# Kernel optimization log

Measured on AMD Instinct MI355X. Metric: run time of the kernel, lower is better.

Reference implementation:

```python
import jax, jax.numpy as jnp
import numpy as np

D_MODEL = 1024
N_HEADS = 16
HEAD_DIM = D_MODEL // N_HEADS
SEQ = 4096
BATCH = 4


def setup_inputs() -> dict:
    key = jax.random.key(0)
    ks = jax.random.split(key, 10)
    s = 0.02
    inp = {
        "h": jax.random.normal(ks[0], (SEQ, BATCH, D_MODEL), jnp.float32),
        "x": jax.random.normal(ks[1], (SEQ, BATCH, D_MODEL), jnp.float32),
        "Wq": jax.random.normal(ks[2], (D_MODEL, D_MODEL), jnp.float32) * s,
        "bq": jnp.zeros((D_MODEL,), jnp.float32),
        "Wk": jax.random.normal(ks[3], (D_MODEL, D_MODEL), jnp.float32) * s,
        "bk": jnp.zeros((D_MODEL,), jnp.float32),
        "Wv": jax.random.normal(ks[4], (D_MODEL, D_MODEL), jnp.float32) * s,
        "bv": jnp.zeros((D_MODEL,), jnp.float32),
        "Wo": jax.random.normal(ks[5], (D_MODEL, D_MODEL), jnp.float32) * s,
        "bo": jnp.zeros((D_MODEL,), jnp.float32),
    }
    return inp


def _heads(t):
    # [S, B, D] -> [B, H, S, d]
    S, B, _ = t.shape
    return t.reshape(S, B, N_HEADS, HEAD_DIM).transpose(1, 2, 0, 3)


def reference(h, x, Wq, bq, Wk, bk, Wv, bv, Wo, bo):
    # torch Linear: y = x @ W.T + b
    Q = _heads(h @ Wq.T + bq)
    K = _heads(x @ Wk.T + bk)
    V = _heads(x @ Wv.T + bv)
    Qp = jax.nn.elu(Q) + 1.0
    Kp = jax.nn.elu(K) + 1.0
    KV = jnp.einsum('bhsd,bhsv->bhdv', Kp, V)          # [B,H,d,d]
    K_sum = Kp.sum(axis=2)                              # [B,H,d]
    Z = jnp.einsum('bhsd,bhd->bhs', Qp, K_sum) + 1e-6   # [B,H,S]
    out = jnp.einsum('bhsd,bhdv->bhsv', Qp, KV) / Z[..., None]
    # [B,H,S,d] -> [S,B,D]
    S, B = h.shape[0], h.shape[1]
    out = out.transpose(2, 0, 1, 3).reshape(S, B, D_MODEL)
    return out @ Wo.T + bo
```

## Files before the change

### kernel.cpp

```cpp
#include <hip/hip_runtime.h>
#include <hip/hip_bf16.h>
#include <cstdint>
#include <cstddef>

#define S_LEN   4096
#define BATCHN  4
#define DMODEL  1024
#define NHEADS  16
#define HDIM    64
#define MROWS   (S_LEN*BATCHN)
#define KDIM    1024
#define NTK     (KDIM/32)
#define CLP     136

typedef __bf16 bf16;
typedef bf16 bf16x8 __attribute__((ext_vector_type(8)));
typedef bf16 bf16x4 __attribute__((ext_vector_type(4)));
typedef float f32x4 __attribute__((ext_vector_type(4)));

#define MFMA16(a,b,c) __builtin_amdgcn_mfma_f32_16x16x32_bf16(a,b,c,0,0,0)

__device__ __forceinline__ void gll16(const void* g, void* l) {
  __builtin_amdgcn_global_load_lds((const __attribute__((address_space(1))) unsigned*)g,
                                   (__attribute__((address_space(3))) unsigned*)l,
                                   16, 0, 0);
}

__global__ __launch_bounds__(256) void cast_perm(const float* __restrict__ h,
                                                 const float* __restrict__ x,
                                                 bf16* __restrict__ hb,
                                                 bf16* __restrict__ xb) {
  const int n = MROWS * KDIM;
  int stride = gridDim.x * blockDim.x * 4;
  for (int i = (blockIdx.x * blockDim.x + threadIdx.x) * 4; i < n; i += stride) {
    int s = i >> 12, b = (i >> 10) & 3, d = i & 1023;
    size_t o = ((size_t)(b * S_LEN + s) << 10) | d;
    float4 f = *(const float4*)(h + i);
    bf16x4 u; u[0]=(bf16)f.x; u[1]=(bf16)f.y; u[2]=(bf16)f.z; u[3]=(bf16)f.w;
    *(bf16x4*)(hb + o) = u;
    float4 g = *(const float4*)(x + i);
    bf16x4 v; v[0]=(bf16)g.x; v[1]=(bf16)g.y; v[2]=(bf16)g.z; v[3]=(bf16)g.w;
    *(bf16x4*)(xb + o) = v;
  }
}

__global__ __launch_bounds__(256) void cast_w(const float* __restrict__ Wq,
                                              const float* __restrict__ Wk,
                                              const float* __restrict__ Wv,
                                              const float* __restrict__ Wo,
                                              bf16* __restrict__ dst) {
  const int n = 4 * 1048576;
  int stride = gridDim.x * blockDim.x * 4;
  for (int i = (blockIdx.x * blockDim.x + threadIdx.x) * 4; i < n; i += stride) {
    int r = i >> 20;
    const float* src = (r < 1) ? (Wq + i) : (r < 2) ? (Wk + i - 1048576)
                     : (r < 3) ? (Wv + i - 2097152) : (Wo + i - 3145728);
    float4 f = *(const float4*)src;
    bf16x4 o; o[0]=(bf16)f.x; o[1]=(bf16)f.y; o[2]=(bf16)f.z; o[3]=(bf16)f.w;
    *(bf16x4*)(dst + i) = o;
  }
}

struct GemmAcc { f32x4 a[4][4]; };

__device__ __forceinline__ void gemm_tile(const bf16* __restrict__ A,
                                          const bf16* __restrict__ Bw,
                                          size_t arow0, size_t brow0,
                                          bf16* sm, GemmAcc& G) {
  const int tid  = threadIdx.x;
  const int wid  = tid >> 6;
  const int lane = tid & 63;
  const int wm = wid >> 1, wn = wid & 1;
  const int lr = lane >> 2;
  const int lc = lane & 3;
  const int ssrc = (((lc << 4) ^ (((lr >> 1) & 3) << 4)) >> 1);
  const int fhalf = (lane >> 4) << 4;

  const bf16* ap[2]; const bf16* bp[2]; int sdo[2];
  #pragma unroll
  for (int i = 0; i < 2; ++i) {
    int seg = (wid << 1) | i;
    ap[i] = A  + (arow0 + seg*16 + lr) * KDIM + ssrc;
    bp[i] = Bw + (brow0 + seg*16 + lr) * KDIM + ssrc;
    sdo[i] = seg * 512;
  }

  #pragma unroll
  for (int i = 0; i < 2; ++i) { gll16(ap[i],      sm + sdo[i]); gll16(bp[i],      sm + 4096 + sdo[i]); }
  #pragma unroll
  for (int i = 0; i < 2; ++i) { gll16(ap[i] + 32, sm + 8192 + sdo[i]); gll16(bp[i] + 32, sm + 12288 + sdo[i]); }
  asm volatile("s_waitcnt vmcnt(4)" ::: "memory");
  __builtin_amdgcn_s_barrier();
  asm volatile("" ::: "memory");

  int cur = 0;
  for (int t = 0; t < NTK; ++t) {
    const bf16* As = sm + cur * 8192;
    const bf16* Bs = As + 4096;

    bf16x8 af[4], bfv[4];
    #pragma unroll
    for (int m = 0; m < 4; ++m) {
      int R = wm*64 + m*16 + (lane & 15);
      af[m] = *(const bf16x8*)((const char*)As + R*64 + (fhalf ^ (((R >> 1) & 3) << 4)));
    }
    #pragma unroll
    for (int n = 0; n < 4; ++n) {
      int R = wn*64 + n*16 + (lane & 15);
      bfv[n] = *(const bf16x8*)((const char*)Bs + R*64 + (fhalf ^ (((R >> 1) & 3) << 4)));
    }

    if (t + 2 < NTK) {
      int nx2 = cur + 2; if (nx2 >= 3) nx2 -= 3;
      bf16* wbA = sm + nx2 * 8192;
      const int ko = (t + 2) * 32;
      #pragma unroll
      for (int i = 0; i < 2; ++i) {
        gll16(ap[i] + ko, wbA + sdo[i]);
        gll16(bp[i] + ko, wbA + 4096 + sdo[i]);
      }
    }

    #pragma unroll
    for (int m = 0; m < 4; ++m)
      #pragma unroll
      for (int n = 0; n < 4; ++n)
        G.a[m][n] = MFMA16(af[m], bfv[n], G.a[m][n]);

    if (t < NTK - 2)       asm volatile("s_waitcnt vmcnt(4)" ::: "memory");
    else if (t == NTK - 2) asm volatile("s_waitcnt vmcnt(0)" ::: "memory");
    if (t < NTK - 1) {
      __builtin_amdgcn_s_barrier();
      asm volatile("" ::: "memory");
    }
    cur = (cur == 2) ? 0 : cur + 1;
  }
}

template<int MODE>
__global__ __launch_bounds__(256) void gemm_bt(
    const bf16* __restrict__ A, const bf16* __restrict__ Bw,
    const float* __restrict__ bias0,
    void* __restrict__ Cout) {
  __shared__ __align__(16) bf16 sm[3 * 8192];
  const int tid  = threadIdx.x;
  const int wid  = tid >> 6;
  const int lane = tid & 63;
  const int wm = wid >> 1, wn = wid & 1;
  const int mtile = blockIdx.x, ntile = blockIdx.y;

  GemmAcc G = {};
  gemm_tile(A, Bw, (size_t)mtile * 128, (size_t)ntile * 128, sm, G);

  #pragma unroll
  for (int m = 0; m < 4; ++m) {
    int rowb = mtile*128 + wm*64 + m*16 + ((lane >> 4) << 2);
    #pragma unroll
    for (int n = 0; n < 4; ++n) {
      int col = ntile*128 + wn*64 + n*16 + (lane & 15);
      float bias = bias0[col];
      if (MODE == 0) {
        bf16* C = (bf16*)Cout;
        #pragma unroll
        for (int i = 0; i < 4; ++i) {
          float v = G.a[m][n][i] + bias;
          v = (v > 0.f) ? v + 1.f : __expf(v);
          C[(size_t)(rowb+i)*DMODEL + col] = (bf16)v;
        }
      } else {
        float* C = (float*)Cout;
        #pragma unroll
        for (int i = 0; i < 4; ++i)
          C[(size_t)(rowb+i)*DMODEL + col] = G.a[m][n][i] + bias;
      }
    }
  }
}

__global__ __launch_bounds__(512, 4) void kvproj(
    const bf16* __restrict__ Wkv, const bf16* __restrict__ xb,
    const float* __restrict__ bk, const float* __restrict__ bv,
    float* __restrict__ kvb, float* __restrict__ ksb) {
  __shared__ __align__(16) bf16 sm[3 * 12288];
  const int tid  = threadIdx.x;
  const int wid  = tid >> 6;
  const int lane = tid & 63;
  const int wm = wid >> 1, wn = wid & 1;
  const int m = blockIdx.x, ntile = blockIdx.y;
  const int lr = lane >> 2;
  const int lc = lane & 3;
  const int ssrc = (((lc << 4) ^ (((lr >> 1) & 3) << 4)) >> 1);
  const int fhalf = (lane >> 4) << 4;

  const bf16* KA = Wkv + (size_t)(m * 128) * KDIM;
  const bf16* VA = Wkv + (size_t)(1024 + m * 128) * KDIM;
  const bf16* BB = xb + (size_t)(ntile * 128) * KDIM;

  const bf16* ap[2]; const bf16* bp; int sda[2], sdb;
  #pragma unroll
  for (int i = 0; i < 2; ++i) {
    int seg = (wid << 1) | i;
    const bf16* base = (seg < 8) ? KA : VA;
    ap[i] = base + (size_t)((seg & 7) * 16 + lr) * KDIM + ssrc;
    sda[i] = seg * 512;
  }
  bp = BB + (size_t)(wid * 16 + lr) * KDIM + ssrc;
  sdb = 8192 + wid * 512;

  #pragma unroll
  for (int i = 0; i < 2; ++i) gll16(ap[i], sm + sda[i]);
  gll16(bp, sm + sdb);
  #pragma unroll
  for (int i = 0; i < 2; ++i) gll16(ap[i] + 32, sm + 12288 + sda[i]);
  gll16(bp + 32, sm + 12288 + sdb);
  asm volatile("s_waitcnt vmcnt(3)" ::: "memory");
  __builtin_amdgcn_s_barrier();
  asm volatile("" ::: "memory");

  f32x4 acc[4][4] = {};
  int cur = 0;
  for (int t = 0; t < NTK; ++t) {
    const bf16* As = sm + cur * 12288;
    const bf16* Bs = As + 8192;

    bf16x8 af[4], bfv[4];
    #pragma unroll
    for (int mm = 0; mm < 4; ++mm) {
      int R = wm*64 + mm*16 + (lane & 15);
      af[mm] = *(const bf16x8*)((const char*)As + R*64 + (fhalf ^ (((R >> 1) & 3) << 4)));
    }
    #pragma unroll
    for (int nn = 0; nn < 4; ++nn) {
      int R = wn*64 + nn*16 + (lane & 15);
      bfv[nn] = *(const bf16x8*)((const char*)Bs + R*64 + (fhalf ^ (((R >> 1) & 3) << 4)));
    }

    if (t + 2 < NTK) {
      int nx2 = cur + 2; if (nx2 >= 3) nx2 -= 3;
      bf16* wb = sm + nx2 * 12288;
      const int ko = (t + 2) * 32;
      #pragma unroll
      for (int i = 0; i < 2; ++i) gll16(ap[i] + ko, wb + sda[i]);
      gll16(bp + ko, wb + sdb);
    }

    #pragma unroll
    for (int mm = 0; mm < 4; ++mm)
      #pragma unroll
      for (int nn = 0; nn < 4; ++nn)
        acc[mm][nn] = MFMA16(af[mm], bfv[nn], acc[mm][nn]);

    if (t < NTK - 2)       asm volatile("s_waitcnt vmcnt(3)" ::: "memory");
    else if (t == NTK - 2) asm volatile("s_waitcnt vmcnt(0)" ::: "memory");
    if (t < NTK - 1) {
      __builtin_amdgcn_s_barrier();
      asm volatile("" ::: "memory");
    }
    cur = (cur == 2) ? 0 : cur + 1;
  }
  __syncthreads();

  bf16* CL = sm;
  #pragma unroll
  for (int mm = 0; mm < 4; ++mm) {
    #pragma unroll
    for (int i = 0; i < 4; ++i) {
      int ra = wm*64 + mm*16 + ((lane >> 4) << 2) + i;
      float bias = (ra < 128) ? bk[m*128 + ra] : bv[m*128 + ra - 128];
      #pragma unroll
      for (int nn = 0; nn < 4; ++nn) {
        int cb = wn*64 + nn*16 + (lane & 15);
        float v = acc[mm][nn][i] + bias;
        if (ra < 128) v = (v > 0.f) ? v + 1.f : __expf(v);
        CL[ra*CLP + cb] = (bf16)v;
      }
    }
  }
  __syncthreads();

  const int hl = wid >> 2;
  const int ww = wid & 3;
  const int bh = (ntile >> 5) * 16 + 2*m + hl;
  f32x4 acc2[4] = {};
  #pragma unroll
  for (int ks = 0; ks < 4; ++ks) {
    bf16x8 akv = *(const bf16x8*)(CL + (hl*64 + ww*16 + (lane & 15))*CLP + ks*32 + ((lane >> 4) << 3));
    #pragma unroll
    for (int nn = 0; nn < 4; ++nn) {
      bf16x8 bkv = *(const bf16x8*)(CL + (128 + hl*64 + nn*16 + (lane & 15))*CLP + ks*32 + ((lane >> 4) << 3));
      acc2[nn] = MFMA16(akv, bkv, acc2[nn]);
    }
  }
  float* KVh = kvb + (size_t)bh * 4096;
  #pragma unroll
  for (int nn = 0; nn < 4; ++nn)
    #pragma unroll
    for (int i = 0; i < 4; ++i) {
      int dd = ww*16 + ((lane >> 4) << 2) + i;
      int vv = nn*16 + (lane & 15);
      atomicAdd(&KVh[dd*64 + vv], acc2[nn][i]);
    }

  {
    int rid = tid >> 2, part = tid & 3;
    float s = 0.f;
    #pragma unroll
    for (int j = 0; j < 32; ++j) s += (float)CL[rid*CLP + part*32 + j];
    s += __shfl_xor(s, 1);
    s += __shfl_xor(s, 2);
    if (part == 0) {
      int hh = rid >> 6, d = rid & 63;
      atomicAdd(&ksb[((ntile >> 5) * 16 + 2*m + hh)*64 + d], s);
    }
  }
}

__global__ __launch_bounds__(256) void attn_out(const bf16* __restrict__ QP,
                                                const float* __restrict__ KVg,
                                                const float* __restrict__ Ksumg,
                                                bf16* __restrict__ OP) {
  const int head = blockIdx.x, stile = blockIdx.y;
  const int b = head >> 4, hh = head & 15;
  const int tid = threadIdx.x;
  const int wid = tid >> 6, lane = tid & 63;
  const int s0 = stile * 128;
  __shared__ __align__(16) bf16 Qs[128*64];
  __shared__ __align__(16) bf16 KVt[64*64];
  __shared__ float ksum_s[64];
  __shared__ float rZ[128];

  const float* KVh = KVg + (size_t)head*4096;
  #pragma unroll
  for (int i = 0; i < 16; ++i) {
    int idx = i*256 + tid;
    int dd = idx >> 6, vv = idx & 63;
    KVt[vv*64 + dd] = (bf16)KVh[idx];
  }
  if (tid < 64) ksum_s[tid] = Ksumg[head*64 + tid];
  #pragma unroll
  for (int p = 0; p < 4; ++p) {
    int row = p*32 + wid*8 + (lane >> 3);
    gll16(QP + ((size_t)(b*S_LEN + s0 + row))*DMODEL + hh*64 + ((lane&7)<<3),
          Qs + (p*32 + wid*8)*64);
  }
  __syncthreads();

  if (tid < 128) {
    float z = 0.f;
    #pragma unroll
    for (int dd = 0; dd < 64; ++dd) z += (float)Qs[tid*64 + dd] * ksum_s[dd];
    rZ[tid] = 1.f / (z + 1e-6f);
  }
  __syncthreads();

  f32x4 acc[2][4] = {};
  #pragma unroll
  for (int ksb2 = 0; ksb2 < 2; ++ksb2) {
    bf16x8 af[2], bv[4];
    #pragma unroll
    for (int m = 0; m < 2; ++m)
      af[m] = *(const bf16x8*)(Qs + (wid*32 + m*16 + (lane & 15))*64 + ksb2*32 + ((lane>>4)<<3));
    #pragma unroll
    for (int n = 0; n < 4; ++n)
      bv[n] = *(const bf16x8*)(KVt + (n*16 + (lane & 15))*64 + ksb2*32 + ((lane>>4)<<3));
    #pragma unroll
    for (int m = 0; m < 2; ++m)
      #pragma unroll
      for (int n = 0; n < 4; ++n)
        acc[m][n] = MFMA16(af[m], bv[n], acc[m][n]);
  }

  #pragma unroll
  for (int m = 0; m < 2; ++m)
    #pragma unroll
    for (int n = 0; n < 4; ++n)
      #pragma unroll
      for (int i = 0; i < 4; ++i) {
        int row = wid*32 + m*16 + ((lane >> 4) << 2) + i;
        int vv  = n*16 + (lane & 15);
        float val = acc[m][n][i] * rZ[row];
        OP[((size_t)((s0+row)*BATCHN + b))*DMODEL + hh*64 + vv] = (bf16)val;
      }
}

extern "C" void kernel_launch(void* const* d_in, const int* in_sizes, int n_in,
                              void* d_out, int out_size, void* d_ws, size_t ws_size,
                              hipStream_t stream) {
  const float* h  = (const float*)d_in[0];
  const float* x  = (const float*)d_in[1];
  const float* Wq = (const float*)d_in[2];
  const float* bq = (const float*)d_in[3];
  const float* Wk = (const float*)d_in[4];
  const float* bk = (const float*)d_in[5];
  const float* Wv = (const float*)d_in[6];
  const float* bv = (const float*)d_in[7];
  const float* Wo = (const float*)d_in[8];
  const float* bo = (const float*)d_in[9];

  char* ws = (char*)d_ws;
  bf16*  hb   = (bf16*)(ws);
  bf16*  xb   = (bf16*)(ws + 33554432);
  bf16*  wcat = (bf16*)(ws + 67108864);
  bf16*  wob  = (bf16*)(ws + 73400320);
  bf16*  qp   = (bf16*)(ws + 75497472);
  float* kvb  = (float*)(ws + 109051904);
  float* ksb  = (float*)(ws + 110100480);
  bf16*  op   = (bf16*)(ws + 110116864);

  cast_perm<<<dim3(4096), 256, 0, stream>>>(h, x, hb, xb);
  cast_w<<<dim3(2048), 256, 0, stream>>>(Wq, Wk, Wv, Wo, wcat);

  hipMemsetAsync(kvb, 0, 1048576 + 16384, stream);

  kvproj<<<dim3(8, 128), 512, 0, stream>>>(wcat + 1048576, xb, bk, bv, kvb, ksb);
  gemm_bt<0><<<dim3(128, 8), 256, 0, stream>>>(hb, wcat, bq, qp);
  attn_out<<<dim3(64, 32), 256, 0, stream>>>(qp, kvb, ksb, op);
  gemm_bt<2><<<dim3(128, 8), 256, 0, stream>>>(op, wob, bo, d_out);
}
```

Before: 257.1 us.

## Fold per-head KV state into output weights and fuse normalizer into Q GEMM

Replaces the per-head attention-output kernel with a small GEMM that premultiplies Wo by each batch/head KV matrix, giving a per-batch combined weight. The Q projection epilogue now computes the feature map, the Z normalizer via cross-lane shuffles, and the scaled Qp. The output GEMM then consumes the normalized Q directly with the batch-specific fused weight. This removes the attn_out pass and its intermediate read/write of the activations. In exchange it adds a weight-sized per-batch precompute and rounds KV·Wo to bf16, which changes numerics.

```diff
diff --git a/kernel.cpp b/kernel.cpp
--- a/kernel.cpp
+++ b/kernel.cpp
@@ -137,11 +137,10 @@
   }
 }
 
-template<int MODE>
-__global__ __launch_bounds__(256) void gemm_bt(
+__global__ __launch_bounds__(256) void q_gemm(
     const bf16* __restrict__ A, const bf16* __restrict__ Bw,
-    const float* __restrict__ bias0,
-    void* __restrict__ Cout) {
+    const float* __restrict__ bq, const float* __restrict__ Ksumg,
+    bf16* __restrict__ qs) {
   __shared__ __align__(16) bf16 sm[3 * 8192];
   const int tid  = threadIdx.x;
   const int wid  = tid >> 6;
@@ -152,26 +151,68 @@
   GemmAcc G = {};
   gemm_tile(A, Bw, (size_t)mtile * 128, (size_t)ntile * 128, sm, G);
 
+  const int hgg = (mtile >> 5) * 16 + ntile * 2 + wn;
+  float ksl[4], bql[4];
+  #pragma unroll
+  for (int n = 0; n < 4; ++n) {
+    ksl[n] = Ksumg[hgg*64 + n*16 + (lane & 15)];
+    bql[n] = bq[ntile*128 + wn*64 + n*16 + (lane & 15)];
+  }
+
+  #pragma unroll
+  for (int m = 0; m < 4; ++m) {
+    #pragma unroll
+    for (int i = 0; i < 4; ++i) {
+      int row = mtile*128 + wm*64 + m*16 + ((lane >> 4) << 2) + i;
+      float v[4], zp = 0.f;
+      #pragma unroll
+      for (int n = 0; n < 4; ++n) {
+        float t = G.a[m][n][i] + bql[n];
+        t = (t > 0.f) ? t + 1.f : __expf(t);
+        v[n] = t;
+        zp += t * ksl[n];
+      }
+      zp += __shfl_xor(zp, 1);
+      zp += __shfl_xor(zp, 2);
+      zp += __shfl_xor(zp, 4);
+      zp += __shfl_xor(zp, 8);
+      float rz = 1.f / (zp + 1e-6f);
+      #pragma unroll
+      for (int n = 0; n < 4; ++n) {
+        int col = ntile*128 + wn*64 + n*16 + (lane & 15);
+        qs[(size_t)row*DMODEL + col] = (bf16)(v[n] * rz);
+      }
+    }
+  }
+}
+
+__global__ __launch_bounds__(256) void out_gemm(const bf16* __restrict__ qsA,
+                                                const bf16* __restrict__ B2,
+                                                const float* __restrict__ bo,
+                                                float* __restrict__ Cout) {
+  __shared__ __align__(16) bf16 sm[3 * 8192];
+  const int tid  = threadIdx.x;
+  const int wid  = tid >> 6;
+  const int lane = tid & 63;
+  const int wm = wid >> 1, wn = wid & 1;
+  const int mtile = blockIdx.x, ntile = blockIdx.y;
+  const bf16* Bw = B2 + (size_t)(mtile >> 5) * 1048576;
+
+  GemmAcc G = {};
+  gemm_tile(qsA, Bw, (size_t)mtile * 128, (size_t)ntile * 128, sm, G);
+
   #pragma unroll
   for (int m = 0; m < 4; ++m) {
     int rowb = mtile*128 + wm*64 + m*16 + ((lane >> 4) << 2);
     #pragma unroll
     for (int n = 0; n < 4; ++n) {
       int col = ntile*128 + wn*64 + n*16 + (lane & 15);
-      float bias = bias0[col];
-      if (MODE == 0) {
-        bf16* C = (bf16*)Cout;
-        #pragma unroll
-        for (int i = 0; i < 4; ++i) {
-          float v = G.a[m][n][i] + bias;
-          v = (v > 0.f) ? v + 1.f : __expf(v);
-          C[(size_t)(rowb+i)*DMODEL + col] = (bf16)v;
-        }
-      } else {
-        float* C = (float*)Cout;
-        #pragma unroll
-        for (int i = 0; i < 4; ++i)
-          C[(size_t)(rowb+i)*DMODEL + col] = G.a[m][n][i] + bias;
+      float bias = bo[col];
+      #pragma unroll
+      for (int i = 0; i < 4; ++i) {
+        int g = rowb + i;
+        int orow = ((g & 4095) << 2) | (g >> 12);
+        Cout[(size_t)orow*DMODEL + col] = G.a[m][n][i] + bias;
       }
     }
   }
@@ -315,54 +356,41 @@
   }
 }
 
-__global__ __launch_bounds__(256) void attn_out(const bf16* __restrict__ QP,
-                                                const float* __restrict__ KVg,
-                                                const float* __restrict__ Ksumg,
-                                                bf16* __restrict__ OP) {
-  const int head = blockIdx.x, stile = blockIdx.y;
-  const int b = head >> 4, hh = head & 15;
+__global__ __launch_bounds__(256) void w2_gemm(const bf16* __restrict__ wob,
+                                               const float* __restrict__ kvb,
+                                               bf16* __restrict__ B2) {
+  const int mtile = blockIdx.x, bh = blockIdx.y;
+  const int b = bh >> 4, hh = bh & 15;
   const int tid = threadIdx.x;
   const int wid = tid >> 6, lane = tid & 63;
-  const int s0 = stile * 128;
-  __shared__ __align__(16) bf16 Qs[128*64];
-  __shared__ __align__(16) bf16 KVt[64*64];
-  __shared__ float ksum_s[64];
-  __shared__ float rZ[128];
-
-  const float* KVh = KVg + (size_t)head*4096;
-  #pragma unroll
-  for (int i = 0; i < 16; ++i) {
-    int idx = i*256 + tid;
-    int dd = idx >> 6, vv = idx & 63;
-    KVt[vv*64 + dd] = (bf16)KVh[idx];
-  }
-  if (tid < 64) ksum_s[tid] = Ksumg[head*64 + tid];
-  #pragma unroll
-  for (int p = 0; p < 4; ++p) {
-    int row = p*32 + wid*8 + (lane >> 3);
-    gll16(QP + ((size_t)(b*S_LEN + s0 + row))*DMODEL + hh*64 + ((lane&7)<<3),
-          Qs + (p*32 + wid*8)*64);
+  __shared__ __align__(16) bf16 Wos[128*64];
+  __shared__ __align__(16) bf16 KVs[64*64];
+
+  #pragma unroll
+  for (int it = 0; it < 4; ++it) {
+    int idx = it*256 + tid;
+    int row = idx >> 3, c = (idx & 7) << 3;
+    *(bf16x8*)(Wos + row*64 + c) =
+      *(const bf16x8*)(wob + (size_t)(mtile*128 + row)*DMODEL + hh*64 + c);
+  }
+  const float* KVh = kvb + (size_t)bh * 4096;
+  #pragma unroll
+  for (int it = 0; it < 16; ++it) {
+    int idx = it*256 + tid;
+    KVs[idx] = (bf16)KVh[idx];
   }
   __syncthreads();
 
-  if (tid < 128) {
-    float z = 0.f;
-    #pragma unroll
-    for (int dd = 0; dd < 64; ++dd) z += (float)Qs[tid*64 + dd] * ksum_s[dd];
-    rZ[tid] = 1.f / (z + 1e-6f);
-  }
-  __syncthreads();
-
   f32x4 acc[2][4] = {};
   #pragma unroll
-  for (int ksb2 = 0; ksb2 < 2; ++ksb2) {
+  for (int ks = 0; ks < 2; ++ks) {
     bf16x8 af[2], bv[4];
     #pragma unroll
     for (int m = 0; m < 2; ++m)
-      af[m] = *(const bf16x8*)(Qs + (wid*32 + m*16 + (lane & 15))*64 + ksb2*32 + ((lane>>4)<<3));
+      af[m] = *(const bf16x8*)(Wos + (wid*32 + m*16 + (lane & 15))*64 + ks*32 + ((lane>>4)<<3));
     #pragma unroll
     for (int n = 0; n < 4; ++n)
-      bv[n] = *(const bf16x8*)(KVt + (n*16 + (lane & 15))*64 + ksb2*32 + ((lane>>4)<<3));
+      bv[n] = *(const bf16x8*)(KVs + (n*16 + (lane & 15))*64 + ks*32 + ((lane>>4)<<3));
     #pragma unroll
     for (int m = 0; m < 2; ++m)
       #pragma unroll
@@ -370,16 +398,16 @@
         acc[m][n] = MFMA16(af[m], bv[n], acc[m][n]);
   }
 
+  bf16* B2b = B2 + (size_t)b * 1048576;
   #pragma unroll
   for (int m = 0; m < 2; ++m)
     #pragma unroll
     for (int n = 0; n < 4; ++n)
       #pragma unroll
       for (int i = 0; i < 4; ++i) {
-        int row = wid*32 + m*16 + ((lane >> 4) << 2) + i;
-        int vv  = n*16 + (lane & 15);
-        float val = acc[m][n][i] * rZ[row];
-        OP[((size_t)((s0+row)*BATCHN + b))*DMODEL + hh*64 + vv] = (bf16)val;
+        int orow = mtile*128 + wid*32 + m*16 + ((lane >> 4) << 2) + i;
+        int dd   = n*16 + (lane & 15);
+        B2b[(size_t)orow*DMODEL + hh*64 + dd] = (bf16)acc[m][n][i];
       }
 }
 
@@ -402,10 +430,10 @@
   bf16*  xb   = (bf16*)(ws + 33554432);
   bf16*  wcat = (bf16*)(ws + 67108864);
   bf16*  wob  = (bf16*)(ws + 73400320);
-  bf16*  qp   = (bf16*)(ws + 75497472);
+  bf16*  qs   = (bf16*)(ws + 75497472);
   float* kvb  = (float*)(ws + 109051904);
   float* ksb  = (float*)(ws + 110100480);
-  bf16*  op   = (bf16*)(ws + 110116864);
+  bf16*  B2   = (bf16*)(ws + 110116864);
 
   cast_perm<<<dim3(4096), 256, 0, stream>>>(h, x, hb, xb);
   cast_w<<<dim3(2048), 256, 0, stream>>>(Wq, Wk, Wv, Wo, wcat);
@@ -413,7 +441,7 @@
   hipMemsetAsync(kvb, 0, 1048576 + 16384, stream);
 
   kvproj<<<dim3(8, 128), 512, 0, stream>>>(wcat + 1048576, xb, bk, bv, kvb, ksb);
-  gemm_bt<0><<<dim3(128, 8), 256, 0, stream>>>(hb, wcat, bq, qp);
-  attn_out<<<dim3(64, 32), 256, 0, stream>>>(qp, kvb, ksb, op);
-  gemm_bt<2><<<dim3(128, 8), 256, 0, stream>>>(op, wob, bo, d_out);
-}
+  w2_gemm<<<dim3(8, 64), 256, 0, stream>>>(wob, kvb, B2);
+  q_gemm<<<dim3(128, 8), 256, 0, stream>>>(hb, wcat, bq, ksb, qs);
+  out_gemm<<<dim3(128, 8), 256, 0, stream>>>(qs, B2, bo, (float*)d_out);
+}
```

Result: faster. 242.5 us (-5.7%).
